# Kernel tuning notes

Hardware: AMD Instinct MI355X
Metric: run time of the kernel (lower is better)

Reference implementation:

```python
import jax, jax.numpy as jnp
import numpy as np

N = 50000      # nodes
E = 800000     # edges (before self loops)
D_IN = 128
D_H = 128
NEG_SLOPE = 0.2  # GATv2Conv default


def setup_inputs() -> dict:
    key = jax.random.key(0)
    ks = jax.random.split(key, 32)
    it = iter(range(32))
    def nk():
        return ks[next(it)]
    def p(shape, scale=0.05):
        return jax.random.normal(nk(), shape, jnp.float32) * scale
    inp = {
        "x": jax.random.normal(nk(), (N, D_IN), jnp.float32),
        "edge_index": jax.random.randint(nk(), (2, E), 0, N, jnp.int32),
        "edge_attr": jax.random.uniform(nk(), (E, 1), jnp.float32),
    }
    dims = [(D_IN, D_H), (D_H, D_H), (D_H, D_H)]
    for i, (di, do) in enumerate(dims, 1):
        inp[f"Wl{i}"] = p((di, do))   # lin_l (source)
        inp[f"Wr{i}"] = p((di, do))   # lin_r (target)
        inp[f"We{i}"] = p((1, do))    # lin_edge (edge_dim=1, no bias)
        inp[f"att{i}"] = p((do,))     # attention vector a
        inp[f"b{i}"] = jnp.zeros((do,), jnp.float32)
    inp["Wlin"] = p((D_H, 1))
    inp["blin"] = jnp.zeros((1,), jnp.float32)
    return inp


def _gatv2(x, src, dst, ew, Wl, Wr, We, att, b):
    # GATv2Conv, heads=1: e = a^T LeakyReLU(Wl x_j + Wr x_i + We ea),
    # alpha = segment_softmax(e over dst), out_i = sum_j alpha * Wl x_j + b
    xl = x @ Wl                       # [N, C] source transform
    xr = x @ Wr                       # [N, C] target transform
    ee = ew @ We                      # [E', C] edge embedding
    s = jax.nn.leaky_relu(xl[src] + xr[dst] + ee, NEG_SLOPE)  # [E', C]
    logits = s @ att                  # [E']
    m = jax.ops.segment_max(logits, dst, num_segments=N)
    e = jnp.exp(logits - m[dst])
    denom = jax.ops.segment_sum(e, dst, num_segments=N)
    alpha = e / denom[dst]            # [E'] segment softmax
    out = jax.ops.segment_sum(alpha[:, None] * xl[src], dst, num_segments=N)
    return out + b


def reference(x, edge_index, edge_attr,
              Wl1, Wr1, We1, att1, b1,
              Wl2, Wr2, We2, att2, b2,
              Wl3, Wr3, We3, att3, b3,
              Wlin, blin):
    # edge_weights = 1/edge_attr, zeros -> 1/1e-4
    zero = edge_attr == 0
    ew = jnp.where(zero, 10000.0, 1.0 / jnp.where(zero, 1.0, edge_attr))
    src, dst = edge_index[0], edge_index[1]
    # add self loops with fill_value=0 edge attr
    loop = jnp.arange(N, dtype=src.dtype)
    src = jnp.concatenate([src, loop])
    dst = jnp.concatenate([dst, loop])
    ew = jnp.concatenate([ew, jnp.zeros((N, 1), ew.dtype)])

    h = jax.nn.relu(_gatv2(x, src, dst, ew, Wl1, Wr1, We1, att1, b1))
    h = jax.nn.relu(_gatv2(h, src, dst, ew, Wl2, Wr2, We2, att2, b2))
    h = _gatv2(h, src, dst, ew, Wl3, Wr3, We3, att3, b3)
    return (h @ Wlin + blin).squeeze(-1)   # [N]
```

## Files before the change

kernel.cpp:

```cpp
#include <hip/hip_runtime.h>
#include <math.h>

#define NN 50000
#define EE 800000
#define EP 850000
#define DD 128
#define NEG_SLOPE 0.2f

typedef float f4  __attribute__((ext_vector_type(4)));
typedef float f32x4 __attribute__((ext_vector_type(4)));
typedef short bf16x8 __attribute__((ext_vector_type(8)));
typedef short s4 __attribute__((ext_vector_type(4)));

static __device__ inline short f2bf(float f) {
    unsigned u = __float_as_uint(f);
    unsigned r = (u + 0x7FFFu + ((u >> 16) & 1u)) >> 16;
    return (short)r;
}
static __device__ inline float bf2f(short s) {
    return __uint_as_float(((unsigned)(unsigned short)s) << 16);
}

__global__ void k_hist(const int* __restrict__ ei, int* __restrict__ counts) {
    int e = blockIdx.x * blockDim.x + threadIdx.x;
    if (e >= EP) return;
    int dst = (e < EE) ? ei[EE + e] : (e - EE);
    atomicAdd(&counts[dst], 1);
}

__global__ void k_scan1(const int* __restrict__ counts, int* __restrict__ row_ptr,
                        int* __restrict__ blockSums) {
    __shared__ int wsum[16];
    int t = threadIdx.x;
    int lane = t & 63;
    int wave = t >> 6;
    int g = blockIdx.x * 1024 + t;
    int v = (g < NN) ? counts[g] : 0;

    int s = v;
#pragma unroll
    for (int o = 1; o < 64; o <<= 1) {
        int u = __shfl_up(s, o, 64);
        if (lane >= o) s += u;
    }
    if (lane == 63) wsum[wave] = s;
    __syncthreads();
    if (wave == 0) {
        int ws = (lane < 16) ? wsum[lane] : 0;
#pragma unroll
        for (int o = 1; o < 16; o <<= 1) {
            int u = __shfl_up(ws, o, 64);
            if (lane >= o) ws += u;
        }
        if (lane < 16) wsum[lane] = ws;
    }
    __syncthreads();
    int base = (wave > 0) ? wsum[wave - 1] : 0;
    int incl = base + s;
    if (g < NN) row_ptr[g] = incl - v;
    if (t == 1023) blockSums[blockIdx.x] = incl;
}

__global__ void k_scan2(const int* __restrict__ blockSums, int* __restrict__ blockOffs,
                        int nb, int* __restrict__ row_ptr) {
    if (threadIdx.x == 0 && blockIdx.x == 0) {
        int run = 0;
        for (int i = 0; i < nb; ++i) { blockOffs[i] = run; run += blockSums[i]; }
        row_ptr[NN] = run;
    }
}

__global__ void k_scan3(int* __restrict__ row_ptr, const int* __restrict__ blockOffs) {
    int g = blockIdx.x * 1024 + threadIdx.x;
    if (g < NN) row_ptr[g] += blockOffs[blockIdx.x];
}

__global__ void k_scatter(const int* __restrict__ ei, const float* __restrict__ eattr,
                          const int* __restrict__ row_ptr, int* __restrict__ fill,
                          int* __restrict__ src_sorted, float* __restrict__ ew_sorted) {
    int e = blockIdx.x * blockDim.x + threadIdx.x;
    if (e >= EP) return;
    int s, d; float w;
    if (e < EE) {
        s = ei[e]; d = ei[EE + e];
        float a = eattr[e];
        w = (a == 0.0f) ? 10000.0f : (1.0f / a);
    } else {
        s = d = e - EE;
        w = 0.0f;
    }
    int pos = row_ptr[d] + atomicAdd(&fill[d], 1);
    src_sorted[pos] = s;
    ew_sorted[pos] = w;
}

__global__ void k_wpack(const float* __restrict__ W0, const float* __restrict__ W1,
                        const float* __restrict__ W2, const float* __restrict__ W3,
                        const float* __restrict__ W4, const float* __restrict__ W5,
                        short* __restrict__ dst) {
    int mat = blockIdx.x >> 6;
    int e = ((blockIdx.x & 63) << 8) + threadIdx.x;
    const float* W = (mat == 0) ? W0 : (mat == 1) ? W1 : (mat == 2) ? W2
                   : (mat == 3) ? W3 : (mat == 4) ? W4 : W5;
    int k = e >> 7, c = e & 127;
    float w = W[e];
    short hb = f2bf(w);
    short lb = f2bf(w - bf2f(hb));
    int ks = k >> 5, kk = k & 31, g = kk >> 3, j = kk & 7, ct = c >> 4, cl = c & 15;
    int off = ((ks * 8 + ct) * 64 + (g * 16 + cl)) * 8 + j;
    int base = (mat >> 1) * 65536 + (mat & 1) * 32768;
    dst[base + off] = hb;
    dst[base + 16384 + off] = lb;
}

#define GB_ROWS 128
__global__ __launch_bounds__(256, 2) void k_gemm_mfma(const float* __restrict__ X,
        const short* __restrict__ Wpk,
        float* __restrict__ xl, float* __restrict__ xr, int nrows) {
    __shared__ short xh[128 * 128];
    __shared__ short xlo[128 * 128];
    int t = threadIdx.x;
    int rowbase = blockIdx.x * GB_ROWS;

#pragma unroll
    for (int i = 0; i < 16; ++i) {
        int idx = t + i * 256;
        int r = idx >> 5;
        int k4 = idx & 31;
        f4 v = {0.f, 0.f, 0.f, 0.f};
        int gr = rowbase + r;
        if (gr < nrows) v = *(const f4*)&X[gr * DD + k4 * 4];
        s4 h, l;
#pragma unroll
        for (int j = 0; j < 4; ++j) {
            short hb = f2bf(v[j]);
            h[j] = hb;
            l[j] = f2bf(v[j] - bf2f(hb));
        }
        int si = r * 128 + (((k4 >> 1) ^ (r & 7)) << 3) + (k4 & 1) * 4;
        *(s4*)&xh[si] = h;
        *(s4*)&xlo[si] = l;
    }
    __syncthreads();

    int wave = t >> 6, lane = t & 63;
    int wr = wave >> 1, wc = wave & 1;

    f32x4 acc[4][4][2];
#pragma unroll
    for (int rt = 0; rt < 4; ++rt)
#pragma unroll
        for (int ct = 0; ct < 4; ++ct) {
            acc[rt][ct][0] = (f32x4){0.f, 0.f, 0.f, 0.f};
            acc[rt][ct][1] = (f32x4){0.f, 0.f, 0.f, 0.f};
        }

    for (int ks = 0; ks < 4; ++ks) {
        bf16x8 Ah[4], Al[4];
#pragma unroll
        for (int rt = 0; rt < 4; ++rt) {
            int row = wr * 64 + rt * 16 + (lane & 15);
            int slot = ks * 4 + (lane >> 4);
            int si = row * 128 + ((slot ^ (row & 7)) << 3);
            Ah[rt] = *(const bf16x8*)&xh[si];
            Al[rt] = *(const bf16x8*)&xlo[si];
        }
#pragma unroll
        for (int ct = 0; ct < 4; ++ct) {
            int ctg = wc * 4 + ct;
            int fb = ((ks * 8 + ctg) * 64 + lane) * 8;
            bf16x8 Blh = *(const bf16x8*)&Wpk[fb];
            bf16x8 Bll = *(const bf16x8*)&Wpk[16384 + fb];
            bf16x8 Brh = *(const bf16x8*)&Wpk[32768 + fb];
            bf16x8 Brl = *(const bf16x8*)&Wpk[49152 + fb];
#pragma unroll
            for (int rt = 0; rt < 4; ++rt) {
                acc[rt][ct][0] = __builtin_amdgcn_mfma_f32_16x16x32_bf16(Ah[rt], Blh, acc[rt][ct][0], 0, 0, 0);
                acc[rt][ct][0] = __builtin_amdgcn_mfma_f32_16x16x32_bf16(Ah[rt], Bll, acc[rt][ct][0], 0, 0, 0);
                acc[rt][ct][0] = __builtin_amdgcn_mfma_f32_16x16x32_bf16(Al[rt], Blh, acc[rt][ct][0], 0, 0, 0);
                acc[rt][ct][1] = __builtin_amdgcn_mfma_f32_16x16x32_bf16(Ah[rt], Brh, acc[rt][ct][1], 0, 0, 0);
                acc[rt][ct][1] = __builtin_amdgcn_mfma_f32_16x16x32_bf16(Ah[rt], Brl, acc[rt][ct][1], 0, 0, 0);
                acc[rt][ct][1] = __builtin_amdgcn_mfma_f32_16x16x32_bf16(Al[rt], Brh, acc[rt][ct][1], 0, 0, 0);
            }
        }
    }

#pragma unroll
    for (int rt = 0; rt < 4; ++rt) {
#pragma unroll
        for (int reg = 0; reg < 4; ++reg) {
            int row = rowbase + wr * 64 + rt * 16 + (lane >> 4) * 4 + reg;
            if (row < nrows) {
#pragma unroll
                for (int ct = 0; ct < 4; ++ct) {
                    int col = wc * 64 + ct * 16 + (lane & 15);
                    xl[row * DD + col] = acc[rt][ct][0][reg];
                    xr[row * DD + col] = acc[rt][ct][1][reg];
                }
            }
        }
    }
}

__device__ inline f4 lrelu4(f4 v) {
    f4 r;
    r.x = v.x > 0.f ? v.x : NEG_SLOPE * v.x;
    r.y = v.y > 0.f ? v.y : NEG_SLOPE * v.y;
    r.z = v.z > 0.f ? v.z : NEG_SLOPE * v.z;
    r.w = v.w > 0.f ? v.w : NEG_SLOPE * v.w;
    return r;
}

template<bool DO_RELU, bool FUSE_FINAL>
__global__ __launch_bounds__(256) void k_agg_t(const float* __restrict__ xl,
        const float* __restrict__ xr, const int* __restrict__ row_ptr,
        const int* __restrict__ src_sorted, const float* __restrict__ ew_sorted,
        const float* __restrict__ We, const float* __restrict__ att,
        const float* __restrict__ bias, float* __restrict__ out,
        const float* __restrict__ Wlin, const float* __restrict__ blin,
        float* __restrict__ outS) {
    int wid = (blockIdx.x * blockDim.x + threadIdx.x) >> 6;
    int lane = threadIdx.x & 63;
    if (wid >= NN) return;
    int quarter = lane >> 4;
    int c = (lane & 15) * 8;

    const f4 xrv0 = *(const f4*)&xr[wid * DD + c];
    const f4 xrv1 = *(const f4*)&xr[wid * DD + c + 4];
    const f4 att0 = *(const f4*)&att[c];
    const f4 att1 = *(const f4*)&att[c + 4];
    const f4 We0  = *(const f4*)&We[c];
    const f4 We1  = *(const f4*)&We[c + 4];

    int beg = row_ptr[wid];
    int end = row_ptr[wid + 1];
    int niter = (end - beg + 3) >> 2;

    float m = -1e30f;
    float d = 0.0f;
    f4 acc0 = {0,0,0,0}, acc1 = {0,0,0,0};

    int e0 = beg + quarter;
    bool val_cur = (e0 < end);
    int ee0 = val_cur ? e0 : (end - 1);
    float w_cur = ew_sorted[ee0];
    int s_cur = src_sorted[ee0];
    f4 x0c = *(const f4*)&xl[s_cur * DD + c];
    f4 x1c = *(const f4*)&xl[s_cur * DD + c + 4];

    for (int i = 0; i < niter; ++i) {
        f4 x0n = {0,0,0,0}, x1n = {0,0,0,0};
        float w_nxt = 0.f; bool val_nxt = false;
        if (i + 1 < niter) {
            int e = beg + 4 * (i + 1) + quarter;
            val_nxt = (e < end);
            int ee = val_nxt ? e : (end - 1);
            w_nxt = ew_sorted[ee];
            int sn = src_sorted[ee];
            x0n = *(const f4*)&xl[sn * DD + c];
            x1n = *(const f4*)&xl[sn * DD + c + 4];
        }

        f4 t0 = lrelu4(x0c + xrv0 + w_cur * We0);
        f4 t1 = lrelu4(x1c + xrv1 + w_cur * We1);
        float p = t0.x * att0.x + t0.y * att0.y + t0.z * att0.z + t0.w * att0.w
                + t1.x * att1.x + t1.y * att1.y + t1.z * att1.z + t1.w * att1.w;
#pragma unroll
        for (int o = 8; o >= 1; o >>= 1) p += __shfl_xor(p, o, 64);

        float logit = val_cur ? p : -1e30f;
        float nm = fmaxf(m, logit);
        float sc = __expf(m - nm);
        float pe = __expf(logit - nm);
        d = d * sc + pe;
        acc0 = acc0 * sc + pe * x0c;
        acc1 = acc1 * sc + pe * x1c;
        m = nm;

        x0c = x0n; x1c = x1n; w_cur = w_nxt; val_cur = val_nxt;
    }

#pragma unroll
    for (int o = 16; o <= 32; o <<= 1) {
        float mo = __shfl_xor(m, o, 64);
        float dn = __shfl_xor(d, o, 64);
        f4 a0o, a1o;
        a0o.x = __shfl_xor(acc0.x, o, 64); a0o.y = __shfl_xor(acc0.y, o, 64);
        a0o.z = __shfl_xor(acc0.z, o, 64); a0o.w = __shfl_xor(acc0.w, o, 64);
        a1o.x = __shfl_xor(acc1.x, o, 64); a1o.y = __shfl_xor(acc1.y, o, 64);
        a1o.z = __shfl_xor(acc1.z, o, 64); a1o.w = __shfl_xor(acc1.w, o, 64);
        float M  = fmaxf(m, mo);
        float sA = __expf(m - M);
        float sB = __expf(mo - M);
        d = d * sA + dn * sB;
        acc0 = acc0 * sA + a0o * sB;
        acc1 = acc1 * sA + a1o * sB;
        m = M;
    }

    if (quarter == 0) {
        float inv = 1.0f / d;
        f4 bv0 = *(const f4*)&bias[c];
        f4 bv1 = *(const f4*)&bias[c + 4];
        f4 o0 = acc0 * inv + bv0;
        f4 o1 = acc1 * inv + bv1;
        if (DO_RELU) {
            o0.x = fmaxf(o0.x, 0.f); o0.y = fmaxf(o0.y, 0.f);
            o0.z = fmaxf(o0.z, 0.f); o0.w = fmaxf(o0.w, 0.f);
            o1.x = fmaxf(o1.x, 0.f); o1.y = fmaxf(o1.y, 0.f);
            o1.z = fmaxf(o1.z, 0.f); o1.w = fmaxf(o1.w, 0.f);
        }
        if (FUSE_FINAL) {
            f4 wl0 = *(const f4*)&Wlin[c];
            f4 wl1 = *(const f4*)&Wlin[c + 4];
            float p = o0.x * wl0.x + o0.y * wl0.y + o0.z * wl0.z + o0.w * wl0.w
                    + o1.x * wl1.x + o1.y * wl1.y + o1.z * wl1.z + o1.w * wl1.w;
#pragma unroll
            for (int o = 8; o >= 1; o >>= 1) p += __shfl_xor(p, o, 64);
            if (lane == 0) outS[wid] = p + blin[0];
        } else {
            *(f4*)&out[wid * DD + c] = o0;
            *(f4*)&out[wid * DD + c + 4] = o1;
        }
    }
}

static inline size_t align256(size_t x) { return (x + 255) & ~(size_t)255; }

extern "C" void kernel_launch(void* const* d_in, const int* in_sizes, int n_in,
                              void* d_out, int out_size, void* d_ws, size_t ws_size,
                              hipStream_t stream) {
    const float* x     = (const float*)d_in[0];
    const int*   ei    = (const int*)d_in[1];
    const float* eattr = (const float*)d_in[2];
    const float* Wl[3]  = {(const float*)d_in[3],  (const float*)d_in[8],  (const float*)d_in[13]};
    const float* Wr[3]  = {(const float*)d_in[4],  (const float*)d_in[9],  (const float*)d_in[14]};
    const float* We[3]  = {(const float*)d_in[5],  (const float*)d_in[10], (const float*)d_in[15]};
    const float* att[3] = {(const float*)d_in[6],  (const float*)d_in[11], (const float*)d_in[16]};
    const float* bb[3]  = {(const float*)d_in[7],  (const float*)d_in[12], (const float*)d_in[17]};
    const float* Wlin = (const float*)d_in[18];
    const float* blin = (const float*)d_in[19];

    char* p = (char*)d_ws;
    int* counts = (int*)p;          p += align256((size_t)NN * 4);
    int* fill   = (int*)p;          p += align256((size_t)NN * 4);
    int* row_ptr= (int*)p;          p += align256((size_t)(NN + 1) * 4);
    int* blockSums = (int*)p;       p += align256(64 * 4);
    int* blockOffs = (int*)p;       p += align256(64 * 4);
    int* src_sorted = (int*)p;      p += align256((size_t)EP * 4);
    float* ew_sorted = (float*)p;   p += align256((size_t)EP * 4);
    float* xl = (float*)p;          p += align256((size_t)NN * DD * 4);
    float* xr = (float*)p;          p += align256((size_t)NN * DD * 4);
    float* hA = (float*)p;          p += align256((size_t)NN * DD * 4);
    float* hB = (float*)p;          p += align256((size_t)NN * DD * 4);
    short* wpk = (short*)p;         p += align256((size_t)3 * 65536 * 2);

    hipMemsetAsync(counts, 0, align256((size_t)NN * 4) + align256((size_t)NN * 4), stream);

    const int nb_scan = (NN + 1023) / 1024;
    k_hist<<<(EP + 255) / 256, 256, 0, stream>>>(ei, counts);
    k_scan1<<<nb_scan, 1024, 0, stream>>>(counts, row_ptr, blockSums);
    k_scan2<<<1, 64, 0, stream>>>(blockSums, blockOffs, nb_scan, row_ptr);
    k_scan3<<<nb_scan, 1024, 0, stream>>>(row_ptr, blockOffs);
    k_scatter<<<(EP + 255) / 256, 256, 0, stream>>>(ei, eattr, row_ptr, fill, src_sorted, ew_sorted);

    k_wpack<<<6 * 64, 256, 0, stream>>>(Wl[0], Wr[0], Wl[1], Wr[1], Wl[2], Wr[2], wpk);

    const int gemm_grid = (NN + GB_ROWS - 1) / GB_ROWS;
    const int agg_grid  = (NN + 3) / 4;

    k_gemm_mfma<<<gemm_grid, 256, 0, stream>>>(x, wpk + 0 * 65536, xl, xr, NN);
    k_agg_t<true, false><<<agg_grid, 256, 0, stream>>>(xl, xr, row_ptr, src_sorted, ew_sorted,
                                        We[0], att[0], bb[0], hA, nullptr, nullptr, nullptr);
    k_gemm_mfma<<<gemm_grid, 256, 0, stream>>>(hA, wpk + 1 * 65536, xl, xr, NN);
    k_agg_t<true, false><<<agg_grid, 256, 0, stream>>>(xl, xr, row_ptr, src_sorted, ew_sorted,
                                        We[1], att[1], bb[1], hB, nullptr, nullptr, nullptr);
    k_gemm_mfma<<<gemm_grid, 256, 0, stream>>>(hB, wpk + 2 * 65536, xl, xr, NN);
    k_agg_t<false, true><<<agg_grid, 256, 0, stream>>>(xl, xr, row_ptr, src_sorted, ew_sorted,
                                        We[2], att[2], bb[2], nullptr, Wlin, blin, (float*)d_out);
}
```

Before: 479.6 us.

## Reuse histogram ranks in scatter, shrink GEMM tile, process 8 edges per aggregation step

The histogram kernel now records each edge's atomic rank, so the scatter kernel uses it directly instead of a second atomic pass over a fill array. The GEMM drops from 128-row to 64-row blocks, with each wave covering all rows and a 32-column slice, to get more blocks and higher occupancy. The aggregation kernel splits each wave into 8 groups of 8 lanes, each lane handling 16 channels, so 8 edges are processed per iteration instead of 4. The trade-off is more registers per lane, a larger rank buffer in the workspace, and more reloading of the weights across the extra GEMM blocks.

```diff
diff --git a/kernel.cpp b/kernel.cpp
--- a/kernel.cpp
+++ b/kernel.cpp
@@ -21,11 +21,12 @@
     return __uint_as_float(((unsigned)(unsigned short)s) << 16);
 }
 
-__global__ void k_hist(const int* __restrict__ ei, int* __restrict__ counts) {
+__global__ void k_hist(const int* __restrict__ ei, int* __restrict__ counts,
+                       int* __restrict__ rank) {
     int e = blockIdx.x * blockDim.x + threadIdx.x;
     if (e >= EP) return;
     int dst = (e < EE) ? ei[EE + e] : (e - EE);
-    atomicAdd(&counts[dst], 1);
+    rank[e] = atomicAdd(&counts[dst], 1);
 }
 
 __global__ void k_scan1(const int* __restrict__ counts, int* __restrict__ row_ptr,
@@ -76,7 +77,7 @@
 }
 
 __global__ void k_scatter(const int* __restrict__ ei, const float* __restrict__ eattr,
-                          const int* __restrict__ row_ptr, int* __restrict__ fill,
+                          const int* __restrict__ row_ptr, const int* __restrict__ rank,
                           int* __restrict__ src_sorted, float* __restrict__ ew_sorted) {
     int e = blockIdx.x * blockDim.x + threadIdx.x;
     if (e >= EP) return;
@@ -89,7 +90,7 @@
         s = d = e - EE;
         w = 0.0f;
     }
-    int pos = row_ptr[d] + atomicAdd(&fill[d], 1);
+    int pos = row_ptr[d] + rank[e];
     src_sorted[pos] = s;
     ew_sorted[pos] = w;
 }
@@ -113,17 +114,17 @@
     dst[base + 16384 + off] = lb;
 }
 
-#define GB_ROWS 128
-__global__ __launch_bounds__(256, 2) void k_gemm_mfma(const float* __restrict__ X,
+#define GB_ROWS 64
+__global__ __launch_bounds__(256, 3) void k_gemm_mfma(const float* __restrict__ X,
         const short* __restrict__ Wpk,
         float* __restrict__ xl, float* __restrict__ xr, int nrows) {
-    __shared__ short xh[128 * 128];
-    __shared__ short xlo[128 * 128];
+    __shared__ short xh[64 * 128];
+    __shared__ short xlo[64 * 128];
     int t = threadIdx.x;
     int rowbase = blockIdx.x * GB_ROWS;
 
 #pragma unroll
-    for (int i = 0; i < 16; ++i) {
+    for (int i = 0; i < 8; ++i) {
         int idx = t + i * 256;
         int r = idx >> 5;
         int k4 = idx & 31;
@@ -144,13 +145,12 @@
     __syncthreads();
 
     int wave = t >> 6, lane = t & 63;
-    int wr = wave >> 1, wc = wave & 1;
-
-    f32x4 acc[4][4][2];
+
+    f32x4 acc[4][2][2];
 #pragma unroll
     for (int rt = 0; rt < 4; ++rt)
 #pragma unroll
-        for (int ct = 0; ct < 4; ++ct) {
+        for (int ct = 0; ct < 2; ++ct) {
             acc[rt][ct][0] = (f32x4){0.f, 0.f, 0.f, 0.f};
             acc[rt][ct][1] = (f32x4){0.f, 0.f, 0.f, 0.f};
         }
@@ -159,15 +159,15 @@
         bf16x8 Ah[4], Al[4];
 #pragma unroll
         for (int rt = 0; rt < 4; ++rt) {
-            int row = wr * 64 + rt * 16 + (lane & 15);
+            int row = rt * 16 + (lane & 15);
             int slot = ks * 4 + (lane >> 4);
             int si = row * 128 + ((slot ^ (row & 7)) << 3);
             Ah[rt] = *(const bf16x8*)&xh[si];
             Al[rt] = *(const bf16x8*)&xlo[si];
         }
 #pragma unroll
-        for (int ct = 0; ct < 4; ++ct) {
-            int ctg = wc * 4 + ct;
+        for (int ct = 0; ct < 2; ++ct) {
+            int ctg = wave * 2 + ct;
             int fb = ((ks * 8 + ctg) * 64 + lane) * 8;
             bf16x8 Blh = *(const bf16x8*)&Wpk[fb];
             bf16x8 Bll = *(const bf16x8*)&Wpk[16384 + fb];
@@ -189,11 +189,11 @@
     for (int rt = 0; rt < 4; ++rt) {
 #pragma unroll
         for (int reg = 0; reg < 4; ++reg) {
-            int row = rowbase + wr * 64 + rt * 16 + (lane >> 4) * 4 + reg;
+            int row = rowbase + rt * 16 + (lane >> 4) * 4 + reg;
             if (row < nrows) {
 #pragma unroll
-                for (int ct = 0; ct < 4; ++ct) {
-                    int col = wc * 64 + ct * 16 + (lane & 15);
+                for (int ct = 0; ct < 2; ++ct) {
+                    int col = wave * 32 + ct * 16 + (lane & 15);
                     xl[row * DD + col] = acc[rt][ct][0][reg];
                     xr[row * DD + col] = acc[rt][ct][1][reg];
                 }
@@ -209,6 +209,9 @@
     r.z = v.z > 0.f ? v.z : NEG_SLOPE * v.z;
     r.w = v.w > 0.f ? v.w : NEG_SLOPE * v.w;
     return r;
+}
+__device__ inline float dot4(f4 a, f4 b) {
+    return a.x * b.x + a.y * b.y + a.z * b.z + a.w * b.w;
 }
 
 template<bool DO_RELU, bool FUSE_FINAL>
@@ -222,105 +225,117 @@
     int wid = (blockIdx.x * blockDim.x + threadIdx.x) >> 6;
     int lane = threadIdx.x & 63;
     if (wid >= NN) return;
-    int quarter = lane >> 4;
-    int c = (lane & 15) * 8;
-
-    const f4 xrv0 = *(const f4*)&xr[wid * DD + c];
-    const f4 xrv1 = *(const f4*)&xr[wid * DD + c + 4];
-    const f4 att0 = *(const f4*)&att[c];
-    const f4 att1 = *(const f4*)&att[c + 4];
-    const f4 We0  = *(const f4*)&We[c];
-    const f4 We1  = *(const f4*)&We[c + 4];
+    int grp = lane >> 3;
+    int c = (lane & 7) * 16;
+
+    f4 xrv[4], attv[4], Wev[4];
+#pragma unroll
+    for (int j = 0; j < 4; ++j) {
+        xrv[j]  = *(const f4*)&xr[wid * DD + c + 4 * j];
+        attv[j] = *(const f4*)&att[c + 4 * j];
+        Wev[j]  = *(const f4*)&We[c + 4 * j];
+    }
 
     int beg = row_ptr[wid];
     int end = row_ptr[wid + 1];
-    int niter = (end - beg + 3) >> 2;
+    int niter = (end - beg + 7) >> 3;
 
     float m = -1e30f;
     float d = 0.0f;
-    f4 acc0 = {0,0,0,0}, acc1 = {0,0,0,0};
-
-    int e0 = beg + quarter;
+    f4 acc[4];
+#pragma unroll
+    for (int j = 0; j < 4; ++j) acc[j] = (f4){0.f, 0.f, 0.f, 0.f};
+
+    int e0 = beg + grp;
     bool val_cur = (e0 < end);
     int ee0 = val_cur ? e0 : (end - 1);
     float w_cur = ew_sorted[ee0];
     int s_cur = src_sorted[ee0];
-    f4 x0c = *(const f4*)&xl[s_cur * DD + c];
-    f4 x1c = *(const f4*)&xl[s_cur * DD + c + 4];
+    f4 xc[4];
+#pragma unroll
+    for (int j = 0; j < 4; ++j) xc[j] = *(const f4*)&xl[s_cur * DD + c + 4 * j];
 
     for (int i = 0; i < niter; ++i) {
-        f4 x0n = {0,0,0,0}, x1n = {0,0,0,0};
+        f4 xn[4];
+#pragma unroll
+        for (int j = 0; j < 4; ++j) xn[j] = (f4){0.f, 0.f, 0.f, 0.f};
         float w_nxt = 0.f; bool val_nxt = false;
         if (i + 1 < niter) {
-            int e = beg + 4 * (i + 1) + quarter;
+            int e = beg + 8 * (i + 1) + grp;
             val_nxt = (e < end);
             int ee = val_nxt ? e : (end - 1);
             w_nxt = ew_sorted[ee];
             int sn = src_sorted[ee];
-            x0n = *(const f4*)&xl[sn * DD + c];
-            x1n = *(const f4*)&xl[sn * DD + c + 4];
-        }
-
-        f4 t0 = lrelu4(x0c + xrv0 + w_cur * We0);
-        f4 t1 = lrelu4(x1c + xrv1 + w_cur * We1);
-        float p = t0.x * att0.x + t0.y * att0.y + t0.z * att0.z + t0.w * att0.w
-                + t1.x * att1.x + t1.y * att1.y + t1.z * att1.z + t1.w * att1.w;
-#pragma unroll
-        for (int o = 8; o >= 1; o >>= 1) p += __shfl_xor(p, o, 64);
+#pragma unroll
+            for (int j = 0; j < 4; ++j) xn[j] = *(const f4*)&xl[sn * DD + c + 4 * j];
+        }
+
+        float p = 0.f;
+#pragma unroll
+        for (int j = 0; j < 4; ++j)
+            p += dot4(lrelu4(xc[j] + xrv[j] + w_cur * Wev[j]), attv[j]);
+#pragma unroll
+        for (int o = 4; o >= 1; o >>= 1) p += __shfl_xor(p, o, 64);
 
         float logit = val_cur ? p : -1e30f;
         float nm = fmaxf(m, logit);
         float sc = __expf(m - nm);
         float pe = __expf(logit - nm);
         d = d * sc + pe;
-        acc0 = acc0 * sc + pe * x0c;
-        acc1 = acc1 * sc + pe * x1c;
+#pragma unroll
+        for (int j = 0; j < 4; ++j) acc[j] = acc[j] * sc + pe * xc[j];
         m = nm;
 
-        x0c = x0n; x1c = x1n; w_cur = w_nxt; val_cur = val_nxt;
-    }
-
-#pragma unroll
-    for (int o = 16; o <= 32; o <<= 1) {
+#pragma unroll
+        for (int j = 0; j < 4; ++j) xc[j] = xn[j];
+        w_cur = w_nxt; val_cur = val_nxt;
+    }
+
+#pragma unroll
+    for (int o = 8; o <= 32; o <<= 1) {
         float mo = __shfl_xor(m, o, 64);
         float dn = __shfl_xor(d, o, 64);
-        f4 a0o, a1o;
-        a0o.x = __shfl_xor(acc0.x, o, 64); a0o.y = __shfl_xor(acc0.y, o, 64);
-        a0o.z = __shfl_xor(acc0.z, o, 64); a0o.w = __shfl_xor(acc0.w, o, 64);
-        a1o.x = __shfl_xor(acc1.x, o, 64); a1o.y = __shfl_xor(acc1.y, o, 64);
-        a1o.z = __shfl_xor(acc1.z, o, 64); a1o.w = __shfl_xor(acc1.w, o, 64);
+        f4 ao[4];
+#pragma unroll
+        for (int j = 0; j < 4; ++j) {
+            ao[j].x = __shfl_xor(acc[j].x, o, 64);
+            ao[j].y = __shfl_xor(acc[j].y, o, 64);
+            ao[j].z = __shfl_xor(acc[j].z, o, 64);
+            ao[j].w = __shfl_xor(acc[j].w, o, 64);
+        }
         float M  = fmaxf(m, mo);
         float sA = __expf(m - M);
         float sB = __expf(mo - M);
         d = d * sA + dn * sB;
-        acc0 = acc0 * sA + a0o * sB;
-        acc1 = acc1 * sA + a1o * sB;
+#pragma unroll
+        for (int j = 0; j < 4; ++j) acc[j] = acc[j] * sA + ao[j] * sB;
         m = M;
     }
 
-    if (quarter == 0) {
+    if (grp == 0) {
         float inv = 1.0f / d;
-        f4 bv0 = *(const f4*)&bias[c];
-        f4 bv1 = *(const f4*)&bias[c + 4];
-        f4 o0 = acc0 * inv + bv0;
-        f4 o1 = acc1 * inv + bv1;
-        if (DO_RELU) {
-            o0.x = fmaxf(o0.x, 0.f); o0.y = fmaxf(o0.y, 0.f);
-            o0.z = fmaxf(o0.z, 0.f); o0.w = fmaxf(o0.w, 0.f);
-            o1.x = fmaxf(o1.x, 0.f); o1.y = fmaxf(o1.y, 0.f);
-            o1.z = fmaxf(o1.z, 0.f); o1.w = fmaxf(o1.w, 0.f);
+        f4 o[4];
+#pragma unroll
+        for (int j = 0; j < 4; ++j) {
+            f4 bv = *(const f4*)&bias[c + 4 * j];
+            o[j] = acc[j] * inv + bv;
+            if (DO_RELU) {
+                o[j].x = fmaxf(o[j].x, 0.f); o[j].y = fmaxf(o[j].y, 0.f);
+                o[j].z = fmaxf(o[j].z, 0.f); o[j].w = fmaxf(o[j].w, 0.f);
+            }
         }
         if (FUSE_FINAL) {
-            f4 wl0 = *(const f4*)&Wlin[c];
-            f4 wl1 = *(const f4*)&Wlin[c + 4];
-            float p = o0.x * wl0.x + o0.y * wl0.y + o0.z * wl0.z + o0.w * wl0.w
-                    + o1.x * wl1.x + o1.y * wl1.y + o1.z * wl1.z + o1.w * wl1.w;
-#pragma unroll
-            for (int o = 8; o >= 1; o >>= 1) p += __shfl_xor(p, o, 64);
+            float p = 0.f;
+#pragma unroll
+            for (int j = 0; j < 4; ++j)
+                p += dot4(o[j], *(const f4*)&Wlin[c + 4 * j]);
+#pragma unroll
+            for (int oo = 4; oo >= 1; oo >>= 1) p += __shfl_xor(p, oo, 64);
             if (lane == 0) outS[wid] = p + blin[0];
         } else {
-            *(f4*)&out[wid * DD + c] = o0;
-            *(f4*)&out[wid * DD + c + 4] = o1;
+#pragma unroll
+            for (int j = 0; j < 4; ++j)
+                *(f4*)&out[wid * DD + c + 4 * j] = o[j];
         }
     }
 }
@@ -343,7 +358,7 @@
 
     char* p = (char*)d_ws;
     int* counts = (int*)p;          p += align256((size_t)NN * 4);
-    int* fill   = (int*)p;          p += align256((size_t)NN * 4);
+    int* rank   = (int*)p;          p += align256((size_t)EP * 4);
     int* row_ptr= (int*)p;          p += align256((size_t)(NN + 1) * 4);
     int* blockSums = (int*)p;       p += align256(64 * 4);
     int* blockOffs = (int*)p;       p += align256(64 * 4);
@@ -355,14 +370,14 @@
     float* hB = (float*)p;          p += align256((size_t)NN * DD * 4);
     short* wpk = (short*)p;         p += align256((size_t)3 * 65536 * 2);
 
-    hipMemsetAsync(counts, 0, align256((size_t)NN * 4) + align256((size_t)NN * 4), stream);
+    hipMemsetAsync(counts, 0, (size_t)NN * 4, stream);
 
     const int nb_scan = (NN + 1023) / 1024;
-    k_hist<<<(EP + 255) / 256, 256, 0, stream>>>(ei, counts);
+    k_hist<<<(EP + 255) / 256, 256, 0, stream>>>(ei, counts, rank);
     k_scan1<<<nb_scan, 1024, 0, stream>>>(counts, row_ptr, blockSums);
     k_scan2<<<1, 64, 0, stream>>>(blockSums, blockOffs, nb_scan, row_ptr);
     k_scan3<<<nb_scan, 1024, 0, stream>>>(row_ptr, blockOffs);
-    k_scatter<<<(EP + 255) / 256, 256, 0, stream>>>(ei, eattr, row_ptr, fill, src_sorted, ew_sorted);
+    k_scatter<<<(EP + 255) / 256, 256, 0, stream>>>(ei, eattr, row_ptr, rank, src_sorted, ew_sorted);
 
     k_wpack<<<6 * 64, 256, 0, stream>>>(Wl[0], Wr[0], Wl[1], Wr[1], Wl[2], Wr[2], wpk);
 
```

Result: slower. 513.7 us (+7.1%).
